# Optimization experiments

Measured on AMD Instinct MI355X. Metric: run time of the kernel, lower is better.

## Reference

```python
import jax, jax.numpy as jnp
import numpy as np

DEPTH, HEADS, DIM_HEAD = 6, 8, 64
B, N, E = 2, 128, 160
NUM_ATOMS, NF = 100, 127
DIM = NF + 1                 # 128, node feature dim fed to transformer
INNER = HEADS * DIM_HEAD     # 512


def setup_inputs() -> dict:
    key = jax.random.key(0)
    ks = iter(jax.random.split(key, 40))
    f32 = jnp.float32
    def w(shape, scale=0.02):
        return jax.random.normal(next(ks), shape, dtype=f32) * scale
    inp = {
        "indices": jax.random.randint(next(ks), (B, N), 0, NUM_ATOMS),
        "coordinates": jax.random.normal(next(ks), (B, N, 3), dtype=f32),
        "bonds": jax.random.randint(next(ks), (E, 2), 0, N),
        "noise_level": jax.random.uniform(next(ks), (1,), dtype=f32),
        "atom_emb": w((NUM_ATOMS, NF), 1.0),
        "ln1_g": jnp.ones((DEPTH, DIM), f32), "ln1_b": jnp.zeros((DEPTH, DIM), f32),
        "Wq": w((DEPTH, DIM, INNER)), "bq": jnp.zeros((DEPTH, INNER), f32),
        "Wkv": w((DEPTH, DIM, 2 * INNER)), "bkv": jnp.zeros((DEPTH, 2 * INNER), f32),
        "We": w((DEPTH, 3, INNER)), "be": jnp.zeros((DEPTH, INNER), f32),
        "Wo": w((DEPTH, INNER, DIM)), "bo": jnp.zeros((DEPTH, DIM), f32),
        "Wg1": w((DEPTH, 3 * DIM, 1)),
        "ln2_g": jnp.ones((DEPTH, DIM), f32), "ln2_b": jnp.zeros((DEPTH, DIM), f32),
        "W1": w((DEPTH, DIM, 4 * DIM)), "b1": jnp.zeros((DEPTH, 4 * DIM), f32),
        "W2": w((DEPTH, 4 * DIM, DIM)), "b2": jnp.zeros((DEPTH, DIM), f32),
        "Wg2": w((DEPTH, 3 * DIM, 1)),
        "Wlin": w((DIM, 1)), "blin": jnp.zeros((1,), f32),
    }
    return inp


def _ln(x, g, b, eps=1e-5):
    m = jnp.mean(x, -1, keepdims=True)
    v = jnp.mean((x - m) ** 2, -1, keepdims=True)
    return (x - m) * jax.lax.rsqrt(v + eps) * g + b


def _gated_residual(x, res, Wg):
    # gate = sigmoid(Linear([x, res, x-res])); out = x*gate + res*(1-gate)
    gate = jax.nn.sigmoid(jnp.concatenate([x, res, x - res], -1) @ Wg)  # (B,N,1)
    return x * gate + res * (1.0 - gate)


def _forward(indices, bonds, coordinates, noise_level, atom_emb,
             ln1_g, ln1_b, Wq, bq, Wkv, bkv, We, be, Wo, bo, Wg1,
             ln2_g, ln2_b, W1, b1, W2, b2, Wg2, Wlin, blin):
    b, n = indices.shape
    # nodes_embedding: atom embedding + noise-level channel
    noise = jnp.broadcast_to(noise_level.reshape(1, 1, 1).astype(coordinates.dtype), (b, n, 1))
    nodes = jnp.concatenate([atom_emb[indices], noise], -1)  # (B,N,DIM)
    # edges_embedding: vectorized scatter of per-bond coordinate differences
    i, j = bonds[:, 0], bonds[:, 1]
    diff = coordinates[:, i] - coordinates[:, j]             # (B,E,3)
    edges = jnp.zeros((b, n, n, 3), coordinates.dtype)
    edges = edges.at[:, i, j].set(diff).at[:, j, i].set(-diff)

    scale = DIM_HEAD ** -0.5
    for l in range(DEPTH):
        # PreNorm + edge-biased attention (mask is all-ones -> no-op)
        xn = _ln(nodes, ln1_g[l], ln1_b[l])
        q = (xn @ Wq[l] + bq[l]).reshape(b, n, HEADS, DIM_HEAD)
        k, v = jnp.split(xn @ Wkv[l] + bkv[l], 2, -1)
        k = k.reshape(b, n, HEADS, DIM_HEAD)
        v = v.reshape(b, n, HEADS, DIM_HEAD)
        e = (edges @ We[l] + be[l]).reshape(b, n, n, HEADS, DIM_HEAD)
        kk = k[:, None] + e                                   # (B,i,j,H,D)
        vv = v[:, None] + e
        sim = jnp.einsum('bihd,bijhd->bijh', q, kk) * scale
        attn = jax.nn.softmax(sim, axis=2)                    # softmax over j
        out = jnp.einsum('bijh,bijhd->bihd', attn, vv).reshape(b, n, INNER)
        out = out @ Wo[l] + bo[l]
        nodes = _gated_residual(out, nodes, Wg1[l])
        # PreNorm + FeedForward (exact GELU, mult=4) + gated residual
        xn = _ln(nodes, ln2_g[l], ln2_b[l])
        ff = jax.nn.gelu(xn @ W1[l] + b1[l], approximate=False) @ W2[l] + b2[l]
        nodes = _gated_residual(ff, nodes, Wg2[l])
    return jnp.sum(nodes @ Wlin + blin)


def reference(indices, coordinates, bonds, noise_level, atom_emb,
              ln1_g, ln1_b, Wq, bq, Wkv, bkv, We, be, Wo, bo, Wg1,
              ln2_g, ln2_b, W1, b1, W2, b2, Wg2, Wlin, blin):
    return _forward(indices, bonds, coordinates, noise_level, atom_emb,
                    ln1_g, ln1_b, Wq, bq, Wkv, bkv, We, be, Wo, bo, Wg1,
                    ln2_g, ln2_b, W1, b1, W2, b2, Wg2, Wlin, blin)
```

## Files before the change

### kernel.cpp

```cpp
#include <hip/hip_runtime.h>
#include <hip/hip_fp16.h>
#include <math.h>

#define DEPTH 6
#define NN    128
#define EE    160
#define NF    127
#define DIMM  128
#define INNER 512
#define NNODE 256

typedef _Float16 h2f16 __attribute__((ext_vector_type(2)));

#if defined(__has_builtin)
#if __has_builtin(__builtin_amdgcn_fdot2)
#define HAVE_FDOT2 1
#endif
#endif

__device__ __forceinline__ float fdot2f(h2f16 a, h2f16 b, float c) {
#ifdef HAVE_FDOT2
    return __builtin_amdgcn_fdot2(a, b, c, false);
#else
    return c + (float)a.x * (float)b.x + (float)a.y * (float)b.y;
#endif
}

__device__ __forceinline__ void gload16(const void* g, void* l) {
    __builtin_amdgcn_global_load_lds((const __attribute__((address_space(1))) void*)g,
                                     (__attribute__((address_space(3))) void*)l,
                                     16, 0, 0);
}

template <int N>
__device__ __forceinline__ void wait_vm() {
    __builtin_amdgcn_s_waitcnt((0xF << 8) | (7 << 4) | (N & 0xF) | ((N >> 4) << 14));
}
__device__ __forceinline__ void wait_lgkm0() { __builtin_amdgcn_s_waitcnt(0xC07F); }
__device__ __forceinline__ void sbar0() { __builtin_amdgcn_sched_barrier(0); }

__device__ __forceinline__ void stage8c(const char* g, char* lds, int ln) {
#pragma unroll
    for (int i = 0; i < 8; i++)
        gload16(g + i * 1024 + ln * 16, lds + i * 1024);
}
__device__ __forceinline__ void stage8f(const char* g, int rs, char* lds, int ln) {
#pragma unroll
    for (int i = 0; i < 8; i++)
        gload16(g + (size_t)i * rs + ln * 16, lds + i * 1024);
}


template <int NXT>
__device__ __forceinline__ float gemv512v2(const __half* s_xh, float* wbuf,
                                           const char* nextG, int ln) {
    const char* Wb = (const char*)wbuf;
    float4 wa[8], wb[8];
    wait_vm<8>();
#pragma unroll
    for (int i = 0; i < 8; i++) wa[i] = *(const float4*)(Wb + i * 1024 + ln * 16);
    sbar0(); wait_lgkm0(); sbar0();
    if (NXT) { stage8c(nextG, (char*)wbuf, ln); wait_vm<8>(); }
    else     wait_vm<0>();
#pragma unroll
    for (int i = 0; i < 8; i++) wb[i] = *(const float4*)(Wb + 8192 + i * 1024 + ln * 16);
    sbar0(); wait_lgkm0(); sbar0();
    if (NXT) stage8c(nextG + 8192, (char*)wbuf + 8192, ln);
    const float4* X = (const float4*)s_xh;
    float a0 = 0, a1 = 0, a2 = 0, a3 = 0;
#pragma unroll
    for (int i = 0; i < 8; i++) {
        float4 xv = X[i];
        const h2f16* wh = (const h2f16*)&wa[i];
        const h2f16* xh = (const h2f16*)&xv;
        a0 = fdot2f(xh[0], wh[0], a0); a1 = fdot2f(xh[1], wh[1], a1);
        a2 = fdot2f(xh[2], wh[2], a2); a3 = fdot2f(xh[3], wh[3], a3);
    }
#pragma unroll
    for (int i = 0; i < 8; i++) {
        float4 xv = X[8 + i];
        const h2f16* wh = (const h2f16*)&wb[i];
        const h2f16* xh = (const h2f16*)&xv;
        a0 = fdot2f(xh[0], wh[0], a0); a1 = fdot2f(xh[1], wh[1], a1);
        a2 = fdot2f(xh[2], wh[2], a2); a3 = fdot2f(xh[3], wh[3], a3);
    }
    return (a0 + a1) + (a2 + a3);
}

template <int NXT>
__device__ __forceinline__ float gemv128v2(const __half* s_xp, float* wbuf,
                                           const char* nextG, int ln) {
    const char* Wb = (const char*)wbuf;
    const char* Xb = (const char*)s_xp + (ln & 3) * 272;
    float4 wa[8], wb[8];
    wait_vm<8>();
#pragma unroll
    for (int i = 0; i < 8; i++) wa[i] = *(const float4*)(Wb + i * 1024 + ln * 16);
    sbar0(); wait_lgkm0(); sbar0();
    if (NXT) { stage8c(nextG, (char*)wbuf, ln); wait_vm<8>(); }
    else     wait_vm<0>();
#pragma unroll
    for (int i = 0; i < 8; i++) wb[i] = *(const float4*)(Wb + 8192 + i * 1024 + ln * 16);
    sbar0(); wait_lgkm0(); sbar0();
    if (NXT) stage8c(nextG + 8192, (char*)wbuf + 8192, ln);
    float a0 = 0, a1 = 0, a2 = 0, a3 = 0;
#pragma unroll
    for (int i = 0; i < 8; i++) {
        float4 xv = *(const float4*)(Xb + i * 16);
        const h2f16* wh = (const h2f16*)&wa[i];
        const h2f16* xh = (const h2f16*)&xv;
        a0 = fdot2f(xh[0], wh[0], a0); a1 = fdot2f(xh[1], wh[1], a1);
        a2 = fdot2f(xh[2], wh[2], a2); a3 = fdot2f(xh[3], wh[3], a3);
    }
#pragma unroll
    for (int i = 0; i < 8; i++) {
        float4 xv = *(const float4*)(Xb + 128 + i * 16);
        const h2f16* wh = (const h2f16*)&wb[i];
        const h2f16* xh = (const h2f16*)&xv;
        a0 = fdot2f(xh[0], wh[0], a0); a1 = fdot2f(xh[1], wh[1], a1);
        a2 = fdot2f(xh[2], wh[2], a2); a3 = fdot2f(xh[3], wh[3], a3);
    }
    return (a0 + a1) + (a2 + a3);
}

template <int NXT>
__device__ __forceinline__ float4 gemvf32(const float* s_xn, float* wbuf,
                                          const char* nextG, int nrs, int w, int ln) {
    const float4* w4 = (const float4*)wbuf;
    float4 wr[16];
    wait_vm<8>();
#pragma unroll
    for (int r = 0; r < 8; r++) wr[r] = w4[r * 64 + ln];
    sbar0(); wait_lgkm0(); sbar0();
    if (NXT) { stage8f(nextG, nrs, (char*)wbuf, ln); wait_vm<8>(); }
    else     wait_vm<0>();
#pragma unroll
    for (int r = 8; r < 16; r++) wr[r] = w4[r * 64 + ln];
    sbar0(); wait_lgkm0(); sbar0();
    if (NXT) stage8f(nextG + (size_t)8 * nrs, nrs, (char*)wbuf + 8192, ln);
    float4 acc = {0, 0, 0, 0};
#pragma unroll
    for (int r = 0; r < 16; r++) {
        float a = s_xn[w * 16 + r];
        acc.x += a * wr[r].x; acc.y += a * wr[r].y;
        acc.z += a * wr[r].z; acc.w += a * wr[r].w;
    }
    return acc;
}

template <int N>
__device__ __forceinline__ void block_reduce_n(float* vals, float* sbuf) {
#pragma unroll
    for (int off = 32; off > 0; off >>= 1)
#pragma unroll
        for (int q = 0; q < N; q++) vals[q] += __shfl_xor(vals[q], off, 64);
    int wave = threadIdx.x >> 6;
    if ((threadIdx.x & 63) == 0)
#pragma unroll
        for (int q = 0; q < N; q++) sbuf[wave * N + q] = vals[q];
    __syncthreads();
#pragma unroll
    for (int q = 0; q < N; q++) {
        float r = 0.0f;
#pragma unroll
        for (int g = 0; g < 8; g++) r += sbuf[g * N + q];
        vals[q] = r;
    }
    __syncthreads();
}

__device__ __forceinline__ float gelu_exact(float a) {
    return 0.5f * a * (1.0f + erff(a * 0.70710678f));
}

__global__ __launch_bounds__(512, 1) void k_pre(
        const int* indices, const float* coords, const int* bonds, const float* noise,
        const float* atom_emb, const float* ln1_g, const float* ln1_b,
        const float* Wq, const float* bq, const float* Wkv, const float* bkv,
        const float* Wo, const float* W1, const float* W2,
        __half* hWq, __half* hWkv, __half* hWo, __half* hW1, __half* hW2,
        float* nodes, float* qb, __half* hk, __half* hv, float* sedgews,
        const float* blin, float* out) {
    int bn = blockIdx.x;
    int b = bn >> 7, i = bn & 127;
    int t  = threadIdx.x;
    int d  = t & 127;
    bool own = (t < 128);
    int w = t >> 6, ln = t & 63;
    __shared__ float arena[32768];
    __shared__ float scoord[384];
    __shared__ int   sadj[128];
    __shared__ float s_xn[128];
    __shared__ float s_red[48];
    __shared__ float s_part[2048];
    float* wbuf = arena + w * 4096;
    char*  wbufc = (char*)wbuf;

    if (bn == 0 && t == 0) out[0] = 256.0f * blin[0];

    const char* phB[6] = {(const char*)Wq,            (const char*)Wq + 1024,
                          (const char*)Wkv,           (const char*)Wkv + 1024,
                          (const char*)Wkv + 2048,    (const char*)Wkv + 3072};
    const int phRS[6] = {2048, 2048, 4096, 4096, 4096, 4096};

    stage8f(phB[0] + (size_t)(w * 16) * phRS[0], phRS[0], wbufc, ln);
    stage8f(phB[0] + (size_t)(w * 16 + 8) * phRS[0], phRS[0], wbufc + 8192, ln);

    if (t < 3 * NN) scoord[t] = coords[b * 3 * NN + t];
    if (t < NN) sadj[t] = 0;
    __syncthreads();
    if (t < EE) {
        int e0 = bonds[2 * t], e1 = bonds[2 * t + 1];
        if (e0 == i) sadj[e1] = 1;
        if (e1 == i) sadj[e0] = 1;
    }
    __syncthreads();
    if (t < NN) {
        int j = t;
        float msk = sadj[j] ? 1.0f : 0.0f;
        sedgews[bn * 384 + 3 * j + 0] = msk * (scoord[3 * i + 0] - scoord[3 * j + 0]);
        sedgews[bn * 384 + 3 * j + 1] = msk * (scoord[3 * i + 1] - scoord[3 * j + 1]);
        sedgews[bn * 384 + 3 * j + 2] = msk * (scoord[3 * i + 2] - scoord[3 * j + 2]);
    }

    float nd = 0.0f;
    if (own) {
        int idx = indices[bn];
        nd = (d < NF) ? atom_emb[idx * NF + d] : noise[0];
        nodes[bn * DIMM + d] = nd;
    }
    {
        float vals[2] = {own ? nd : 0.0f, own ? nd * nd : 0.0f};
        block_reduce_n<2>(vals, s_red);
        float m   = vals[0] * (1.0f / 128.0f);
        float var = vals[1] * (1.0f / 128.0f) - m * m;
        if (own) s_xn[d] = (nd - m) * rsqrtf(var + 1e-5f) * ln1_g[d] + ln1_b[d];
    }

    for (int u = bn * 512 + t; u < 294912; u += NNODE * 512) {
        int s = u >> 13, within = u & 8191;
        int l = s / 6, m = s % 6;
        const float* src; __half* dst; int ncols, colofs, big;
        if (m == 0)      { src = Wq  + (size_t)l * 65536;  dst = hWq  + (size_t)l * 65536;         ncols = 512;  colofs = 0;   big = 0; }
        else if (m == 1) { src = Wkv + (size_t)l * 131072; dst = hWkv + (size_t)l * 131072;        ncols = 1024; colofs = 0;   big = 0; }
        else if (m == 2) { src = Wkv + (size_t)l * 131072; dst = hWkv + (size_t)l * 131072 + 65536;ncols = 1024; colofs = 512; big = 0; }
        else if (m == 3) { src = W1  + (size_t)l * 65536;  dst = hW1  + (size_t)l * 65536;         ncols = 512;  colofs = 0;   big = 0; }
        else if (m == 4) { src = Wo  + (size_t)l * 65536;  dst = hWo  + (size_t)l * 65536;         ncols = 128;  colofs = 0;   big = 1; }
        else             { src = W2  + (size_t)l * 65536;  dst = hW2  + (size_t)l * 65536;         ncols = 128;  colofs = 0;   big = 1; }
        int rb, col;
        if (!big) { rb = within >> 9; col = within & 511; }
        else      { rb = within >> 7; col = within & 127; }
        int row0 = rb * 8;
        __align__(16) __half tmp[8];
#pragma unroll
        for (int e = 0; e < 8; e++)
            tmp[e] = __float2half(src[(size_t)(row0 + e) * ncols + colofs + col]);
        int dh;
        if (!big) dh = (col >> 6) * 8192 + rb * 512 + (col & 63) * 8;
        else {
            int kq = row0 >> 7, ci = (row0 & 127) >> 3;
            dh = (col >> 4) * 8192 + ci * 512 + ((col & 15) * 4 + kq) * 8;
        }
        *(float4*)&dst[dh] = *(const float4*)tmp;
    }
    __syncthreads();

#define PRE_COMBINE(P)                                                        \
    {                                                                         \
        ((float4*)(s_part + w * 256))[ln] = acc;                              \
        __syncthreads();                                                      \
        if (t < 256) {                                                        \
            float sS = 0.0f;                                                  \
            _Pragma("unroll")                                                 \
            for (int g = 0; g < 8; g++) sS += s_part[g * 256 + t];            \
            int col = ((P) & 1) * 256 + t;                                    \
            if ((P) < 2)      qb[(size_t)bn * INNER + col] = sS + bq[col];    \
            else if ((P) < 4) hk[(size_t)bn * INNER + col] =                  \
                                  __float2half(sS + bkv[col]);                \
            else              hv[(size_t)bn * INNER + col] =                  \
                                  __float2half(sS + bkv[INNER + col]);        \
        }                                                                     \
        __syncthreads();                                                      \
    }

    {
        float4 acc;
        acc = gemvf32<1>(s_xn, wbuf, phB[1] + (size_t)(w * 16) * phRS[1], phRS[1], w, ln);
        PRE_COMBINE(0);
        acc = gemvf32<1>(s_xn, wbuf, phB[2] + (size_t)(w * 16) * phRS[2], phRS[2], w, ln);
        PRE_COMBINE(1);
        acc = gemvf32<1>(s_xn, wbuf, phB[3] + (size_t)(w * 16) * phRS[3], phRS[3], w, ln);
        PRE_COMBINE(2);
        acc = gemvf32<1>(s_xn, wbuf, phB[4] + (size_t)(w * 16) * phRS[4], phRS[4], w, ln);
        PRE_COMBINE(3);
        acc = gemvf32<1>(s_xn, wbuf, phB[5] + (size_t)(w * 16) * phRS[5], phRS[5], w, ln);
        PRE_COMBINE(4);
        acc = gemvf32<0>(s_xn, wbuf, nullptr, 0, w, ln);
        PRE_COMBINE(5);
    }
#undef PRE_COMBINE
}

__global__ __launch_bounds__(512, 1) void k_layer(int l,
        const float* sedgews,
        const float* We, const float* be,
        float* qb, const __half* hkin, const __half* hvin,
        __half* hkout, __half* hvout,
        const __half* hWo, const float* bo, const float* Wg1,
        const float* ln2_g, const float* ln2_b,
        const __half* hW1, const float* b1,
        const __half* hW2, const float* b2,
        const float* Wg2,
        const float* ln1_g, const float* ln1_b,
        const __half* hWq, const float* bq,
        const __half* hWkv, const float* bkv,
        float* nodes, const float* Wlin, float* out) {
    int bn = blockIdx.x;
    int b = bn >> 7;
    int t = threadIdx.x;
    int d = t & 127;
    bool own = (t < 128);
    int w = t >> 6, ln = t & 63;

    __shared__ float arena[32768];
    __shared__ float sedge[384];
    __shared__ float s_l[64];
    __shared__ __align__(16) __half s_aoh[544];
    __shared__ __align__(16) __half s_hh[544];
    __shared__ __align__(16) __half s_xh[128];
    __shared__ float s_x[128];
    __shared__ float s_red[48];
    __shared__ float s_part[4096];
    float* s_o = s_part;
    float* wbuf = arena + w * 4096;

    const char* WoL  = (const char*)hWo + (size_t)l * 131072 + w * 16384;
    const char* W1L  = (const char*)hW1 + (size_t)l * 131072 + w * 16384;
    const char* W2L  = (const char*)hW2 + (size_t)l * 131072 + w * 16384;
    const char* WqnL = (const char*)hWq + (size_t)(l + 1) * 131072 + w * 16384;
    const char* WknL = (const char*)hWkv + (size_t)(l + 1) * 262144 + w * 16384;
    const char* WvnL = (const char*)hWkv + (size_t)(l + 1) * 262144 + 131072 + w * 16384;

    stage8c(WoL, (char*)wbuf, ln);
    stage8c(WoL + 8192, (char*)wbuf + 8192, ln);

    const float4* qR4 = (const float4*)(qb + (size_t)bn * INNER);
    const float4* WeR = (const float4*)(We + (size_t)l * 3 * INNER);
    float4 qa  = qR4[ln * 2],        qz  = qR4[ln * 2 + 1];
    float4 w0a = WeR[ln * 2],        w0z = WeR[ln * 2 + 1];
    float4 w1a = WeR[128 + ln * 2],  w1z = WeR[129 + ln * 2];
    float4 w2a = WeR[256 + ln * 2],  w2z = WeR[257 + ln * 2];
    float4 bea = ((const float4*)(be + (size_t)l * INNER))[ln * 2];
    float4 bez = ((const float4*)(be + (size_t)l * INNER))[ln * 2 + 1];
    float res = own ? nodes[bn * DIMM + d] : 0.0f;
    h2f16 qh0 = {(_Float16)qa.x, (_Float16)qa.y};
    h2f16 qh1 = {(_Float16)qa.z, (_Float16)qa.w};
    h2f16 qh2 = {(_Float16)qz.x, (_Float16)qz.y};
    h2f16 qh3 = {(_Float16)qz.z, (_Float16)qz.w};
    float c = qa.x * bea.x + qa.y * bea.y + qa.z * bea.z + qa.w * bea.w
            + qz.x * bez.x + qz.y * bez.y + qz.z * bez.z + qz.w * bez.w;
    c += __shfl_xor(c, 1, 64); c += __shfl_xor(c, 2, 64); c += __shfl_xor(c, 4, 64);

    if (t < 384) sedge[t] = sedgews[bn * 384 + t];
    __syncthreads();

    const float4* kR = (const float4*)(hkin + (size_t)b * NN * INNER);
    const float4* vR = (const float4*)(hvin + (size_t)b * NN * INNER);
    float l_run = 0.0f, S_nb = 0.0f;
    float4 o0 = {0, 0, 0, 0}, o1 = {0, 0, 0, 0};
    int j0 = w * 16;
#pragma unroll
    for (int base = 0; base < 16; base += 4) {
        float4 kraw[4], vraw[4];
#pragma unroll
        for (int p = 0; p < 4; p++) {
            int j = j0 + base + p;
            kraw[p] = kR[j * 64 + ln];
            vraw[p] = vR[j * 64 + ln];
        }
#pragma unroll
        for (int p = 0; p < 4; p++) {
            int j = j0 + base + p;
            const h2f16* kh = (const h2f16*)&kraw[p];
            float s = fdot2f(qh0, kh[0],
                      fdot2f(qh1, kh[1],
                      fdot2f(qh2, kh[2],
                      fdot2f(qh3, kh[3], 0.0f))));
            float ex = sedge[3 * j], ey = sedge[3 * j + 1], ez = sedge[3 * j + 2];
            bool bonded = (ex != 0.0f) || (ey != 0.0f) || (ez != 0.0f);
            float4 e0, e1;
            if (bonded) {
                e0.x = bea.x + ex * w0a.x + ey * w1a.x + ez * w2a.x;
                e0.y = bea.y + ex * w0a.y + ey * w1a.y + ez * w2a.y;
                e0.z = bea.z + ex * w0a.z + ey * w1a.z + ez * w2a.z;
                e0.w = bea.w + ex * w0a.w + ey * w1a.w + ez * w2a.w;
                e1.x = bez.x + ex * w0z.x + ey * w1z.x + ez * w2z.x;
                e1.y = bez.y + ex * w0z.y + ey * w1z.y + ez * w2z.y;
                e1.z = bez.z + ex * w0z.z + ey * w1z.z + ez * w2z.z;
                e1.w = bez.w + ex * w0z.w + ey * w1z.w + ez * w2z.w;
                s += qa.x * e0.x + qa.y * e0.y + qa.z * e0.z + qa.w * e0.w
                   + qz.x * e1.x + qz.y * e1.y + qz.z * e1.z + qz.w * e1.w;
            }
            s += __shfl_xor(s, 1, 64);
            s += __shfl_xor(s, 2, 64);
            s += __shfl_xor(s, 4, 64);
            if (!bonded) s += c;
            float pp = __expf(s * 0.125f);
            l_run += pp;
            const __half2* vh = (const __half2*)&vraw[p];
            float2 v0 = __half22float2(vh[0]), v1 = __half22float2(vh[1]);
            float2 v2 = __half22float2(vh[2]), v3 = __half22float2(vh[3]);
            o0.x += pp * v0.x; o0.y += pp * v0.y; o0.z += pp * v1.x; o0.w += pp * v1.y;
            o1.x += pp * v2.x; o1.y += pp * v2.y; o1.z += pp * v3.x; o1.w += pp * v3.y;
            if (bonded) {
                o0.x += pp * e0.x; o0.y += pp * e0.y; o0.z += pp * e0.z; o0.w += pp * e0.w;
                o1.x += pp * e1.x; o1.y += pp * e1.y; o1.z += pp * e1.z; o1.w += pp * e1.w;
            } else S_nb += pp;
        }
    }
    o0.x += S_nb * bea.x; o0.y += S_nb * bea.y; o0.z += S_nb * bea.z; o0.w += S_nb * bea.w;
    o1.x += S_nb * bez.x; o1.y += S_nb * bez.y; o1.z += S_nb * bez.z; o1.w += S_nb * bez.w;
    ((float4*)(s_o + w * 512))[ln * 2]     = o0;
    ((float4*)(s_o + w * 512))[ln * 2 + 1] = o1;
    if ((ln & 7) == 0) s_l[w * 8 + (ln >> 3)] = l_run;
    __syncthreads();
    {
        float o = 0.0f;
#pragma unroll
        for (int g = 0; g < 8; g++) o += s_o[g * 512 + t];
        int h = t >> 6;
        float lsum = 0.0f;
#pragma unroll
        for (int g = 0; g < 8; g++) lsum += s_l[g * 8 + h];
        s_aoh[(t >> 7) * 136 + (t & 127)] = __float2half(o / lsum);
    }
    __syncthreads();

    {
        float xo = gemv128v2<1>(s_aoh, wbuf, W1L, ln);
        xo += __shfl_xor(xo, 1, 64);
        xo += __shfl_xor(xo, 2, 64);
        if ((ln & 3) == 0) s_x[w * 16 + (ln >> 2)] = xo;
    }
    __syncthreads();
    float x = own ? s_x[d] + bo[l * DIMM + d] : 0.0f;

    const float* Wg1_l = Wg1 + l * 3 * DIMM;
    float n1;
    {
        float tex = own ? (x * Wg1_l[d] + res * Wg1_l[DIMM + d]
                           + (x - res) * Wg1_l[2 * DIMM + d]) : 0.0f;
        float vals[6] = {tex,
                         own ? x : 0.0f, own ? x * x : 0.0f,
                         own ? x * res : 0.0f,
                         own ? res : 0.0f, own ? res * res : 0.0f};
        block_reduce_n<6>(vals, s_red);
        float g1 = 1.0f / (1.0f + __expf(-vals[0]));
        float sn  = g1 * vals[1] + (1.0f - g1) * vals[4];
        float sn2 = g1 * g1 * vals[2] + 2.0f * g1 * (1.0f - g1) * vals[3]
                  + (1.0f - g1) * (1.0f - g1) * vals[5];
        float m   = sn * (1.0f / 128.0f);
        float var = sn2 * (1.0f / 128.0f) - m * m;
        n1 = x * g1 + res * (1.0f - g1);
        if (own) s_xh[d] = __float2half((n1 - m) * rsqrtf(var + 1e-5f) * ln2_g[l * DIMM + d]
                                        + ln2_b[l * DIMM + d]);
    }
    __syncthreads();

    {
        float a1 = gemv512v2<1>(s_xh, wbuf, W2L, ln);
        int col = w * 64 + ln;
        float ag = gelu_exact(a1 + b1[l * 4 * DIMM + col]);
        s_hh[(col >> 7) * 136 + (col & 127)] = __float2half(ag);
    }
    __syncthreads();

    {
        float yw;
        if (l < DEPTH - 1) yw = gemv128v2<1>(s_hh, wbuf, WqnL, ln);
        else               yw = gemv128v2<0>(s_hh, wbuf, nullptr, ln);
        yw += __shfl_xor(yw, 1, 64);
        yw += __shfl_xor(yw, 2, 64);
        if ((ln & 3) == 0) s_x[w * 16 + (ln >> 2)] = yw;
    }
    __syncthreads();
    float y = own ? s_x[d] + b2[l * DIMM + d] : 0.0f;

    const float* Wg2_l = Wg2 + l * 3 * DIMM;
    if (l < DEPTH - 1) {
        float tex = own ? (y * Wg2_l[d] + n1 * Wg2_l[DIMM + d]
                           + (y - n1) * Wg2_l[2 * DIMM + d]) : 0.0f;
        float vals[6] = {tex,
                         own ? y : 0.0f, own ? y * y : 0.0f,
                         own ? y * n1 : 0.0f,
                         own ? n1 : 0.0f, own ? n1 * n1 : 0.0f};
        block_reduce_n<6>(vals, s_red);
        float g2 = 1.0f / (1.0f + __expf(-vals[0]));
        float sn  = g2 * vals[1] + (1.0f - g2) * vals[4];
        float sn2 = g2 * g2 * vals[2] + 2.0f * g2 * (1.0f - g2) * vals[3]
                  + (1.0f - g2) * (1.0f - g2) * vals[5];
        float m   = sn * (1.0f / 128.0f);
        float var = sn2 * (1.0f / 128.0f) - m * m;
        float n2 = y * g2 + n1 * (1.0f - g2);
        if (own) {
            nodes[bn * DIMM + d] = n2;
            s_xh[d] = __float2half((n2 - m) * rsqrtf(var + 1e-5f) * ln1_g[(l + 1) * DIMM + d]
                                   + ln1_b[(l + 1) * DIMM + d]);
        }
        __syncthreads();

        int col = w * 64 + ln;
        {
            float q = gemv512v2<1>(s_xh, wbuf, WknL, ln);
            qb[(size_t)bn * INNER + col] = q + bq[(l + 1) * INNER + col];
        }
        {
            float kk = gemv512v2<1>(s_xh, wbuf, WvnL, ln);
            hkout[(size_t)bn * INNER + col] =
                __float2half(kk + bkv[(l + 1) * 2 * INNER + col]);
        }
        {
            float vv = gemv512v2<0>(s_xh, wbuf, nullptr, ln);
            hvout[(size_t)bn * INNER + col] =
                __float2half(vv + bkv[(l + 1) * 2 * INNER + INNER + col]);
        }
    } else {
        float wl = own ? Wlin[d] : 0.0f;
        float tex = own ? (y * Wg2_l[d] + n1 * Wg2_l[DIMM + d]
                           + (y - n1) * Wg2_l[2 * DIMM + d]) : 0.0f;
        float vals[3] = {tex, y * wl, n1 * wl};
        block_reduce_n<3>(vals, s_red);
        float g2 = 1.0f / (1.0f + __expf(-vals[0]));
        float tot = g2 * vals[1] + (1.0f - g2) * vals[2];
        if (t == 0) atomicAdd(out, tot);
    }
}

extern "C" void kernel_launch(void* const* d_in, const int* in_sizes, int n_in,
                              void* d_out, int out_size, void* d_ws, size_t ws_size,
                              hipStream_t stream) {
    const int*   indices = (const int*)d_in[0];
    const float* coords  = (const float*)d_in[1];
    const int*   bonds   = (const int*)d_in[2];
    const float* noise   = (const float*)d_in[3];
    const float* atom_emb= (const float*)d_in[4];
    const float* ln1_g   = (const float*)d_in[5];
    const float* ln1_b   = (const float*)d_in[6];
    const float* Wq      = (const float*)d_in[7];
    const float* bq      = (const float*)d_in[8];
    const float* Wkv     = (const float*)d_in[9];
    const float* bkv     = (const float*)d_in[10];
    const float* We      = (const float*)d_in[11];
    const float* be      = (const float*)d_in[12];
    const float* Wo      = (const float*)d_in[13];
    const float* bo      = (const float*)d_in[14];
    const float* Wg1     = (const float*)d_in[15];
    const float* ln2_g   = (const float*)d_in[16];
    const float* ln2_b   = (const float*)d_in[17];
    const float* W1      = (const float*)d_in[18];
    const float* b1      = (const float*)d_in[19];
    const float* W2      = (const float*)d_in[20];
    const float* b2      = (const float*)d_in[21];
    const float* Wg2     = (const float*)d_in[22];
    const float* Wlin    = (const float*)d_in[23];
    const float* blin    = (const float*)d_in[24];

    float*  ws    = (float*)d_ws;
    float*  nodes = ws;
    float*  qb    = nodes + NNODE * DIMM;
    __half* hkb   = (__half*)(qb + NNODE * INNER);
    __half* hvb   = hkb + 2 * NNODE * INNER;
    __half* hWq   = hvb + 2 * NNODE * INNER;
    __half* hWkv  = hWq + DEPTH * DIMM * INNER;
    __half* hWo   = hWkv + DEPTH * DIMM * 2 * INNER;
    __half* hW1   = hWo + DEPTH * INNER * DIMM;
    __half* hW2   = hW1 + DEPTH * DIMM * 4 * DIMM;
    float*  sedgews = (float*)(hW2 + DEPTH * 4 * DIMM * DIMM);

    k_pre<<<NNODE, 512, 0, stream>>>(indices, coords, bonds, noise, atom_emb,
                                     ln1_g, ln1_b, Wq, bq, Wkv, bkv, Wo, W1, W2,
                                     hWq, hWkv, hWo, hW1, hW2,
                                     nodes, qb, hkb, hvb, sedgews, blin, (float*)d_out);
    for (int l = 0; l < DEPTH; l++) {
        const __half* hkin = hkb + (size_t)(l & 1) * NNODE * INNER;
        const __half* hvin = hvb + (size_t)(l & 1) * NNODE * INNER;
        __half* hkout = hkb + (size_t)((l + 1) & 1) * NNODE * INNER;
        __half* hvout = hvb + (size_t)((l + 1) & 1) * NNODE * INNER;
        k_layer<<<NNODE, 512, 0, stream>>>(l, sedgews, We, be,
                                           qb, hkin, hvin, hkout, hvout,
                                           hWo, bo, Wg1, ln2_g, ln2_b, hW1, b1, hW2, b2,
                                           Wg2, ln1_g, ln1_b, hWq, bq, hWkv, bkv,
                                           nodes, Wlin, (float*)d_out);
    }
}
```

Baseline: 244.5 us.

## Prefetch GEMV weights into registers instead of async LDS staging

Replaces the global_load_lds staging of weight tiles through a per-wave LDS arena with direct register prefetch. Each GEMV's next weight tile is loaded into a 16-entry float4 register array while the current one is consumed. The first-phase prefetch is also moved later, after the edge and attention work, and a dummy LDS pad array is added, apparently to keep LDS usage and occupancy fixed. This removes the LDS round trip and the manual waitcnt choreography, at the cost of more VGPR pressure, and the later start of the first weight load may expose more latency.

```diff
diff --git a/kernel.cpp b/kernel.cpp
--- a/kernel.cpp
+++ b/kernel.cpp
@@ -26,126 +26,73 @@
 #endif
 }
 
-__device__ __forceinline__ void gload16(const void* g, void* l) {
-    __builtin_amdgcn_global_load_lds((const __attribute__((address_space(1))) void*)g,
-                                     (__attribute__((address_space(3))) void*)l,
-                                     16, 0, 0);
-}
-
-template <int N>
-__device__ __forceinline__ void wait_vm() {
-    __builtin_amdgcn_s_waitcnt((0xF << 8) | (7 << 4) | (N & 0xF) | ((N >> 4) << 14));
-}
-__device__ __forceinline__ void wait_lgkm0() { __builtin_amdgcn_s_waitcnt(0xC07F); }
-__device__ __forceinline__ void sbar0() { __builtin_amdgcn_sched_barrier(0); }
-
-__device__ __forceinline__ void stage8c(const char* g, char* lds, int ln) {
+
+__device__ __forceinline__ void ld8(float4 w[16], const char* g, int ln, int base) {
 #pragma unroll
     for (int i = 0; i < 8; i++)
-        gload16(g + i * 1024 + ln * 16, lds + i * 1024);
-}
-__device__ __forceinline__ void stage8f(const char* g, int rs, char* lds, int ln) {
-#pragma unroll
-    for (int i = 0; i < 8; i++)
-        gload16(g + (size_t)i * rs + ln * 16, lds + i * 1024);
-}
-
-
-template <int NXT>
-__device__ __forceinline__ float gemv512v2(const __half* s_xh, float* wbuf,
-                                           const char* nextG, int ln) {
-    const char* Wb = (const char*)wbuf;
-    float4 wa[8], wb[8];
-    wait_vm<8>();
-#pragma unroll
-    for (int i = 0; i < 8; i++) wa[i] = *(const float4*)(Wb + i * 1024 + ln * 16);
-    sbar0(); wait_lgkm0(); sbar0();
-    if (NXT) { stage8c(nextG, (char*)wbuf, ln); wait_vm<8>(); }
-    else     wait_vm<0>();
-#pragma unroll
-    for (int i = 0; i < 8; i++) wb[i] = *(const float4*)(Wb + 8192 + i * 1024 + ln * 16);
-    sbar0(); wait_lgkm0(); sbar0();
-    if (NXT) stage8c(nextG + 8192, (char*)wbuf + 8192, ln);
-    const float4* X = (const float4*)s_xh;
-    float a0 = 0, a1 = 0, a2 = 0, a3 = 0;
+        w[base + i] = *(const float4*)(g + (size_t)(base + i) * 1024 + ln * 16);
+}
+
+__device__ __forceinline__ void dot8h(const float4 w[16], int base, const float4* X,
+                                      float& a0, float& a1, float& a2, float& a3) {
 #pragma unroll
     for (int i = 0; i < 8; i++) {
-        float4 xv = X[i];
-        const h2f16* wh = (const h2f16*)&wa[i];
+        float4 xv = X[base + i];
+        const h2f16* wh = (const h2f16*)&w[base + i];
         const h2f16* xh = (const h2f16*)&xv;
         a0 = fdot2f(xh[0], wh[0], a0); a1 = fdot2f(xh[1], wh[1], a1);
         a2 = fdot2f(xh[2], wh[2], a2); a3 = fdot2f(xh[3], wh[3], a3);
     }
-#pragma unroll
-    for (int i = 0; i < 8; i++) {
-        float4 xv = X[8 + i];
-        const h2f16* wh = (const h2f16*)&wb[i];
-        const h2f16* xh = (const h2f16*)&xv;
-        a0 = fdot2f(xh[0], wh[0], a0); a1 = fdot2f(xh[1], wh[1], a1);
-        a2 = fdot2f(xh[2], wh[2], a2); a3 = fdot2f(xh[3], wh[3], a3);
-    }
+}
+
+template <int NXT>
+__device__ __forceinline__ float gemv512p(const __half* s_xh, float4 w[16],
+                                          const char* nextG, int ln) {
+    const float4* X = (const float4*)s_xh;
+    float a0 = 0, a1 = 0, a2 = 0, a3 = 0;
+    dot8h(w, 0, X, a0, a1, a2, a3);
+    if (NXT) ld8(w, nextG, ln, 0);
+    dot8h(w, 8, X, a0, a1, a2, a3);
+    if (NXT) ld8(w, nextG, ln, 8);
     return (a0 + a1) + (a2 + a3);
 }
 
 template <int NXT>
-__device__ __forceinline__ float gemv128v2(const __half* s_xp, float* wbuf,
-                                           const char* nextG, int ln) {
-    const char* Wb = (const char*)wbuf;
-    const char* Xb = (const char*)s_xp + (ln & 3) * 272;
-    float4 wa[8], wb[8];
-    wait_vm<8>();
-#pragma unroll
-    for (int i = 0; i < 8; i++) wa[i] = *(const float4*)(Wb + i * 1024 + ln * 16);
-    sbar0(); wait_lgkm0(); sbar0();
-    if (NXT) { stage8c(nextG, (char*)wbuf, ln); wait_vm<8>(); }
-    else     wait_vm<0>();
-#pragma unroll
-    for (int i = 0; i < 8; i++) wb[i] = *(const float4*)(Wb + 8192 + i * 1024 + ln * 16);
-    sbar0(); wait_lgkm0(); sbar0();
-    if (NXT) stage8c(nextG + 8192, (char*)wbuf + 8192, ln);
+__device__ __forceinline__ float gemv128p(const __half* s_xp, float4 w[16],
+                                          const char* nextG, int ln) {
+    const float4* X = (const float4*)((const char*)s_xp + (ln & 3) * 272);
     float a0 = 0, a1 = 0, a2 = 0, a3 = 0;
-#pragma unroll
-    for (int i = 0; i < 8; i++) {
-        float4 xv = *(const float4*)(Xb + i * 16);
-        const h2f16* wh = (const h2f16*)&wa[i];
-        const h2f16* xh = (const h2f16*)&xv;
-        a0 = fdot2f(xh[0], wh[0], a0); a1 = fdot2f(xh[1], wh[1], a1);
-        a2 = fdot2f(xh[2], wh[2], a2); a3 = fdot2f(xh[3], wh[3], a3);
-    }
-#pragma unroll
-    for (int i = 0; i < 8; i++) {
-        float4 xv = *(const float4*)(Xb + 128 + i * 16);
-        const h2f16* wh = (const h2f16*)&wb[i];
-        const h2f16* xh = (const h2f16*)&xv;
-        a0 = fdot2f(xh[0], wh[0], a0); a1 = fdot2f(xh[1], wh[1], a1);
-        a2 = fdot2f(xh[2], wh[2], a2); a3 = fdot2f(xh[3], wh[3], a3);
-    }
+    dot8h(w, 0, X, a0, a1, a2, a3);
+    if (NXT) ld8(w, nextG, ln, 0);
+    dot8h(w, 8, X, a0, a1, a2, a3);
+    if (NXT) ld8(w, nextG, ln, 8);
     return (a0 + a1) + (a2 + a3);
 }
 
+__device__ __forceinline__ void ldf8(float4 w[16], const char* g, int rs, int ln, int base) {
+#pragma unroll
+    for (int r = 0; r < 8; r++)
+        w[base + r] = *(const float4*)(g + (size_t)(base + r) * rs + ln * 16);
+}
 template <int NXT>
-__device__ __forceinline__ float4 gemvf32(const float* s_xn, float* wbuf,
-                                          const char* nextG, int nrs, int w, int ln) {
-    const float4* w4 = (const float4*)wbuf;
-    float4 wr[16];
-    wait_vm<8>();
-#pragma unroll
-    for (int r = 0; r < 8; r++) wr[r] = w4[r * 64 + ln];
-    sbar0(); wait_lgkm0(); sbar0();
-    if (NXT) { stage8f(nextG, nrs, (char*)wbuf, ln); wait_vm<8>(); }
-    else     wait_vm<0>();
-#pragma unroll
-    for (int r = 8; r < 16; r++) wr[r] = w4[r * 64 + ln];
-    sbar0(); wait_lgkm0(); sbar0();
-    if (NXT) stage8f(nextG + (size_t)8 * nrs, nrs, (char*)wbuf + 8192, ln);
-    float4 acc = {0, 0, 0, 0};
-#pragma unroll
-    for (int r = 0; r < 16; r++) {
-        float a = s_xn[w * 16 + r];
-        acc.x += a * wr[r].x; acc.y += a * wr[r].y;
-        acc.z += a * wr[r].z; acc.w += a * wr[r].w;
-    }
-    return acc;
+__device__ __forceinline__ void gemvf32p(const float* s_xn, float4 w[16],
+                                         const char* nextG, int nrs, int wv, int ln,
+                                         float4& acc) {
+    acc = {0, 0, 0, 0};
+#pragma unroll
+    for (int r = 0; r < 8; r++) {
+        float a = s_xn[wv * 16 + r];
+        acc.x += a * w[r].x; acc.y += a * w[r].y;
+        acc.z += a * w[r].z; acc.w += a * w[r].w;
+    }
+    if (NXT) ldf8(w, nextG, nrs, ln, 0);
+#pragma unroll
+    for (int r = 8; r < 16; r++) {
+        float a = s_xn[wv * 16 + r];
+        acc.x += a * w[r].x; acc.y += a * w[r].y;
+        acc.z += a * w[r].z; acc.w += a * w[r].w;
+    }
+    if (NXT) ldf8(w, nextG, nrs, ln, 8);
 }
 
 template <int N>
@@ -187,14 +134,13 @@
     int d  = t & 127;
     bool own = (t < 128);
     int w = t >> 6, ln = t & 63;
-    __shared__ float arena[32768];
     __shared__ float scoord[384];
     __shared__ int   sadj[128];
     __shared__ float s_xn[128];
     __shared__ float s_red[48];
     __shared__ float s_part[2048];
-    float* wbuf = arena + w * 4096;
-    char*  wbufc = (char*)wbuf;
+    __shared__ float lds_pad[24576];
+    if (out == (float*)1) lds_pad[t] = 0.0f;
 
     if (bn == 0 && t == 0) out[0] = 256.0f * blin[0];
 
@@ -202,9 +148,6 @@
                           (const char*)Wkv,           (const char*)Wkv + 1024,
                           (const char*)Wkv + 2048,    (const char*)Wkv + 3072};
     const int phRS[6] = {2048, 2048, 4096, 4096, 4096, 4096};
-
-    stage8f(phB[0] + (size_t)(w * 16) * phRS[0], phRS[0], wbufc, ln);
-    stage8f(phB[0] + (size_t)(w * 16 + 8) * phRS[0], phRS[0], wbufc + 8192, ln);
 
     if (t < 3 * NN) scoord[t] = coords[b * 3 * NN + t];
     if (t < NN) sadj[t] = 0;
@@ -263,6 +206,10 @@
         }
         *(float4*)&dst[dh] = *(const float4*)tmp;
     }
+
+    float4 wr[16];
+    ldf8(wr, phB[0] + (size_t)(w * 16) * phRS[0], phRS[0], ln, 0);
+    ldf8(wr, phB[0] + (size_t)(w * 16) * phRS[0], phRS[0], ln, 8);
     __syncthreads();
 
 #define PRE_COMBINE(P)                                                        \
@@ -285,17 +232,17 @@
 
     {
         float4 acc;
-        acc = gemvf32<1>(s_xn, wbuf, phB[1] + (size_t)(w * 16) * phRS[1], phRS[1], w, ln);
+        gemvf32p<1>(s_xn, wr, phB[1] + (size_t)(w * 16) * phRS[1], phRS[1], w, ln, acc);
         PRE_COMBINE(0);
-        acc = gemvf32<1>(s_xn, wbuf, phB[2] + (size_t)(w * 16) * phRS[2], phRS[2], w, ln);
+        gemvf32p<1>(s_xn, wr, phB[2] + (size_t)(w * 16) * phRS[2], phRS[2], w, ln, acc);
         PRE_COMBINE(1);
-        acc = gemvf32<1>(s_xn, wbuf, phB[3] + (size_t)(w * 16) * phRS[3], phRS[3], w, ln);
+        gemvf32p<1>(s_xn, wr, phB[3] + (size_t)(w * 16) * phRS[3], phRS[3], w, ln, acc);
         PRE_COMBINE(2);
-        acc = gemvf32<1>(s_xn, wbuf, phB[4] + (size_t)(w * 16) * phRS[4], phRS[4], w, ln);
+        gemvf32p<1>(s_xn, wr, phB[4] + (size_t)(w * 16) * phRS[4], phRS[4], w, ln, acc);
         PRE_COMBINE(3);
-        acc = gemvf32<1>(s_xn, wbuf, phB[5] + (size_t)(w * 16) * phRS[5], phRS[5], w, ln);
+        gemvf32p<1>(s_xn, wr, phB[5] + (size_t)(w * 16) * phRS[5], phRS[5], w, ln, acc);
         PRE_COMBINE(4);
-        acc = gemvf32<0>(s_xn, wbuf, nullptr, 0, w, ln);
+        gemvf32p<0>(s_xn, wr, nullptr, 0, w, ln, acc);
         PRE_COMBINE(5);
     }
 #undef PRE_COMBINE
@@ -322,7 +269,6 @@
     bool own = (t < 128);
     int w = t >> 6, ln = t & 63;
 
-    __shared__ float arena[32768];
     __shared__ float sedge[384];
     __shared__ float s_l[64];
     __shared__ __align__(16) __half s_aoh[544];
@@ -331,8 +277,9 @@
     __shared__ float s_x[128];
     __shared__ float s_red[48];
     __shared__ float s_part[4096];
+    __shared__ float lds_pad[24576];
+    if (out == (float*)1) lds_pad[t] = 0.0f;
     float* s_o = s_part;
-    float* wbuf = arena + w * 4096;
 
     const char* WoL  = (const char*)hWo + (size_t)l * 131072 + w * 16384;
     const char* W1L  = (const char*)hW1 + (size_t)l * 131072 + w * 16384;
@@ -340,9 +287,6 @@
     const char* WqnL = (const char*)hWq + (size_t)(l + 1) * 131072 + w * 16384;
     const char* WknL = (const char*)hWkv + (size_t)(l + 1) * 262144 + w * 16384;
     const char* WvnL = (const char*)hWkv + (size_t)(l + 1) * 262144 + 131072 + w * 16384;
-
-    stage8c(WoL, (char*)wbuf, ln);
-    stage8c(WoL + 8192, (char*)wbuf + 8192, ln);
 
     const float4* qR4 = (const float4*)(qb + (size_t)bn * INNER);
     const float4* WeR = (const float4*)(We + (size_t)l * 3 * INNER);
@@ -420,6 +364,11 @@
     }
     o0.x += S_nb * bea.x; o0.y += S_nb * bea.y; o0.z += S_nb * bea.z; o0.w += S_nb * bea.w;
     o1.x += S_nb * bez.x; o1.y += S_nb * bez.y; o1.z += S_nb * bez.z; o1.w += S_nb * bez.w;
+
+    float4 wreg[16];
+    ld8(wreg, WoL, ln, 0);
+    ld8(wreg, WoL, ln, 8);
+
     ((float4*)(s_o + w * 512))[ln * 2]     = o0;
     ((float4*)(s_o + w * 512))[ln * 2 + 1] = o1;
     if ((ln & 7) == 0) s_l[w * 8 + (ln >> 3)] = l_run;
@@ -437,7 +386,7 @@
     __syncthreads();
 
     {
-        float xo = gemv128v2<1>(s_aoh, wbuf, W1L, ln);
+        float xo = gemv128p<1>(s_aoh, wreg, W1L, ln);
         xo += __shfl_xor(xo, 1, 64);
         xo += __shfl_xor(xo, 2, 64);
         if ((ln & 3) == 0) s_x[w * 16 + (ln >> 2)] = xo;
@@ -468,7 +417,7 @@
     __syncthreads();
 
     {
-        float a1 = gemv512v2<1>(s_xh, wbuf, W2L, ln);
+        float a1 = gemv512p<1>(s_xh, wreg, W2L, ln);
         int col = w * 64 + ln;
         float ag = gelu_exact(a1 + b1[l * 4 * DIMM + col]);
         s_hh[(col >> 7) * 136 + (col & 127)] = __float2half(ag);
@@ -477,8 +426,8 @@
 
     {
         float yw;
-        if (l < DEPTH - 1) yw = gemv128v2<1>(s_hh, wbuf, WqnL, ln);
-        else               yw = gemv128v2<0>(s_hh, wbuf, nullptr, ln);
+        if (l < DEPTH - 1) yw = gemv128p<1>(s_hh, wreg, WqnL, ln);
+        else               yw = gemv128p<0>(s_hh, wreg, nullptr, ln);
         yw += __shfl_xor(yw, 1, 64);
         yw += __shfl_xor(yw, 2, 64);
         if ((ln & 3) == 0) s_x[w * 16 + (ln >> 2)] = yw;
@@ -511,16 +460,16 @@
 
         int col = w * 64 + ln;
         {
-            float q = gemv512v2<1>(s_xh, wbuf, WknL, ln);
+            float q = gemv512p<1>(s_xh, wreg, WknL, ln);
             qb[(size_t)bn * INNER + col] = q + bq[(l + 1) * INNER + col];
         }
         {
-            float kk = gemv512v2<1>(s_xh, wbuf, WvnL, ln);
+            float kk = gemv512p<1>(s_xh, wreg, WvnL, ln);
             hkout[(size_t)bn * INNER + col] =
                 __float2half(kk + bkv[(l + 1) * 2 * INNER + col]);
         }
         {
-            float vv = gemv512v2<0>(s_xh, wbuf, nullptr, ln);
+            float vv = gemv512p<0>(s_xh, wreg, nullptr, ln);
             hvout[(size_t)bn * INNER + col] =
                 __float2half(vv + bkv[(l + 1) * 2 * INNER + INNER + col]);
         }
```

Result: faster. 228.9 us (-6.4%).
